# Performance work log

Measured on AMD Instinct MI355X. Metric: run time of the kernel, lower is better.

The kernel has to match this reference:

```python
import jax, jax.numpy as jnp
import numpy as np

B, T, H = 32, 2048, 1024

def setup_inputs() -> dict:
    key = jax.random.key(0)
    k1, k2, k3 = jax.random.split(key, 3)
    gru_output = jax.random.normal(k1, (B, T, H), dtype=jnp.float32)
    # Xavier uniform bounds
    lim_w = float(np.sqrt(6.0 / (H + H)))
    lim_c = float(np.sqrt(6.0 / (H + 1)))
    attention_weights = jax.random.uniform(k2, (H, H), minval=-lim_w, maxval=lim_w, dtype=jnp.float32)
    context_vector = jax.random.uniform(k3, (H, 1), minval=-lim_c, maxval=lim_c, dtype=jnp.float32)
    return {"gru_output": gru_output, "attention_weights": attention_weights, "context_vector": context_vector}

def reference(gru_output, attention_weights, context_vector):
    # score: [B, T, H]
    score = jnp.tanh(jnp.einsum('bth,hk->btk', gru_output, attention_weights))
    # logits: [B, T]
    logits = jnp.einsum('bth,h->bt', score, context_vector[:, 0])
    attn = jax.nn.softmax(logits, axis=1)  # over time dim
    # context: [B, H]
    context = jnp.einsum('bth,bt->bh', gru_output, attn)
    return (context, attn)
```

## Files before the change

kernel.cpp:

```cpp
#include <hip/hip_runtime.h>
#include <hip/hip_bf16.h>
#include <stdint.h>

#define B_DIM 32
#define T_DIM 2048
#define H_DIM 1024
#define M_DIM (B_DIM * T_DIM)
#define K_DIM H_DIM
#define N_DIM H_DIM

#define BM 256
#define BN 256
#define BKT 32
#define NTILES (K_DIM / BKT)
#define DEPTH 3

typedef __attribute__((ext_vector_type(4))) float f32x4;
typedef __attribute__((ext_vector_type(8))) short short8;
typedef __attribute__((ext_vector_type(4))) short short4v;

__device__ __forceinline__ unsigned short f2bf(float x) {
  unsigned u = __float_as_uint(x);
  return (unsigned short)((u + 0x7FFFu + ((u >> 16) & 1u)) >> 16);
}
__device__ __forceinline__ float bf2f(unsigned short h) {
  return __uint_as_float(((unsigned)h) << 16);
}
__device__ __forceinline__ float fast_tanh(float x) {
  float e = __expf(2.f * x);
  return 1.f - 2.f / (e + 1.f);
}
__device__ __forceinline__ int swz(int r, int s) {
  return ((r >> 1) << 7) + (((((r & 1) << 2) | s) ^ ((r >> 1) & 7)) << 4);
}

__global__ void convert_g_kernel(const float* __restrict__ in,
                                 unsigned short* __restrict__ out) {
  size_t nvec = (size_t)M_DIM * K_DIM / 8;
  size_t stride = (size_t)gridDim.x * blockDim.x;
  for (size_t i = (size_t)blockIdx.x * blockDim.x + threadIdx.x; i < nvec;
       i += stride) {
    const float4* p = (const float4*)(in + i * 8);
    float4 u0 = p[0], u1 = p[1];
    short8 s;
    s[0] = (short)f2bf(u0.x); s[1] = (short)f2bf(u0.y);
    s[2] = (short)f2bf(u0.z); s[3] = (short)f2bf(u0.w);
    s[4] = (short)f2bf(u1.x); s[5] = (short)f2bf(u1.y);
    s[6] = (short)f2bf(u1.z); s[7] = (short)f2bf(u1.w);
    *(short8*)(out + i * 8) = s;
  }
}

__global__ void convert_w_kernel(const float* __restrict__ w,
                                 unsigned short* __restrict__ wt) {
  __shared__ float tile[64][65];
  int n0 = blockIdx.x * 64;
  int k0 = blockIdx.y * 64;
  int j = threadIdx.x & 63;
  int i0 = threadIdx.x >> 6;
#pragma unroll
  for (int ii = 0; ii < 16; ++ii) {
    int i = i0 * 16 + ii;
    tile[i][j] = w[(size_t)(k0 + i) * H_DIM + n0 + j];
  }
  __syncthreads();
#pragma unroll
  for (int ii = 0; ii < 16; ++ii) {
    int i = i0 * 16 + ii;
    wt[(size_t)(n0 + i) * H_DIM + k0 + j] = f2bf(tile[j][i]);
  }
}

__global__ __launch_bounds__(512, 2) void gemm_tanh_logits(
    const unsigned short* __restrict__ A,
    const unsigned short* __restrict__ Bt,
    const float* __restrict__ cvec,
    float* __restrict__ logits) {
  __shared__ unsigned short lds[4 * 16384];

  const int tid = threadIdx.x;
  const int wid = tid >> 6;
  const int lane = tid & 63;

  int p = blockIdx.x;
  int logical = (p & 7) * 128 + (p >> 3);
  int mrow = logical >> 2;
  int ncol = logical & 3;

  const unsigned short* Ap = A + (size_t)mrow * BM * K_DIM;
  const unsigned short* Bp = Bt + (size_t)ncol * BN * K_DIM;

  const unsigned short *gA[2], *gB[2];
#pragma unroll
  for (int j = 0; j < 2; ++j) {
    int o = j * 8192 + tid * 16;
    int pr = o >> 7;
    int v = ((o >> 4) & 7) ^ (pr & 7);
    int r = (pr << 1) | (v >> 2);
    int s = v & 3;
    gA[j] = Ap + (size_t)r * K_DIM + s * 8;
    gB[j] = Bp + (size_t)r * K_DIM + s * 8;
  }
  const int ldst0 = wid * 512;
  const int ldst1 = wid * 512 + 4096;

  auto stageA = [&](int tt, int bi) {
    __builtin_amdgcn_global_load_lds(
        (const __attribute__((address_space(1))) unsigned int*)(gA[0] + tt * BKT),
        (__attribute__((address_space(3))) unsigned int*)(lds + bi * 16384 + ldst0),
        16, 0, 0);
    __builtin_amdgcn_global_load_lds(
        (const __attribute__((address_space(1))) unsigned int*)(gA[1] + tt * BKT),
        (__attribute__((address_space(3))) unsigned int*)(lds + bi * 16384 + ldst1),
        16, 0, 0);
  };
  auto stageB = [&](int tt, int bi) {
    __builtin_amdgcn_global_load_lds(
        (const __attribute__((address_space(1))) unsigned int*)(gB[0] + tt * BKT),
        (__attribute__((address_space(3))) unsigned int*)(lds + bi * 16384 + 8192 + ldst0),
        16, 0, 0);
    __builtin_amdgcn_global_load_lds(
        (const __attribute__((address_space(1))) unsigned int*)(gB[1] + tt * BKT),
        (__attribute__((address_space(3))) unsigned int*)(lds + bi * 16384 + 8192 + ldst1),
        16, 0, 0);
  };

  const int wm = wid >> 2;
  const int wn = wid & 3;
  const int fr = lane & 15;
  const int sl = lane >> 4;

  const int aoff = swz(wm * 128 + fr, sl) >> 1;
  const int boff = (swz(wn * 64 + fr, sl) >> 1) + 8192;

  f32x4 acc[8][4];
#pragma unroll
  for (int m = 0; m < 8; ++m)
#pragma unroll
    for (int n = 0; n < 4; ++n) acc[m][n] = (f32x4){0.f, 0.f, 0.f, 0.f};

  stageA(0, 0); stageB(0, 0);
  stageA(1, 1); stageB(1, 1);
  stageA(2, 2); stageB(2, 2);
  asm volatile("s_waitcnt vmcnt(8)" ::: "memory");
  __builtin_amdgcn_s_barrier();

  for (int T = 0; T < NTILES; T += 4) {
#pragma unroll
    for (int u = 0; u < 4; ++u) {
      const int t = T + u;
      const unsigned short* L0 = lds + u * 16384;
      short8 a[4], b[4], a2[4];
#pragma unroll
      for (int m = 0; m < 4; ++m) a[m] = *(const short8*)(L0 + aoff + m * 512);
#pragma unroll
      for (int n = 0; n < 4; ++n) b[n] = *(const short8*)(L0 + boff + n * 512);
      if (t + DEPTH < NTILES) stageA(t + DEPTH, (u + 3) & 3);
      __builtin_amdgcn_sched_barrier(0);
      __builtin_amdgcn_s_barrier();
      asm volatile("s_waitcnt lgkmcnt(0)" ::: "memory");
      __builtin_amdgcn_sched_barrier(0);
      __builtin_amdgcn_s_setprio(1);
#pragma unroll
      for (int m = 0; m < 4; ++m)
#pragma unroll
        for (int n = 0; n < 4; ++n)
          acc[m][n] = __builtin_amdgcn_mfma_f32_16x16x32_bf16(a[m], b[n],
                                                              acc[m][n], 0, 0, 0);
      __builtin_amdgcn_s_setprio(0);
      __builtin_amdgcn_sched_barrier(0);
      __builtin_amdgcn_s_barrier();
#pragma unroll
      for (int m = 0; m < 4; ++m)
        a2[m] = *(const short8*)(L0 + aoff + (m + 4) * 512);
      if (t + DEPTH < NTILES) stageB(t + DEPTH, (u + 3) & 3);
      __builtin_amdgcn_sched_barrier(0);
      __builtin_amdgcn_s_barrier();
      asm volatile("s_waitcnt lgkmcnt(0)" ::: "memory");
      __builtin_amdgcn_sched_barrier(0);
      __builtin_amdgcn_s_setprio(1);
#pragma unroll
      for (int m = 0; m < 4; ++m)
#pragma unroll
        for (int n = 0; n < 4; ++n)
          acc[m + 4][n] = __builtin_amdgcn_mfma_f32_16x16x32_bf16(
              a2[m], b[n], acc[m + 4][n], 0, 0, 0);
      __builtin_amdgcn_s_setprio(0);
      __builtin_amdgcn_sched_barrier(0);
      if (t < NTILES - DEPTH)
        asm volatile("s_waitcnt vmcnt(8)" ::: "memory");
      else if (t == NTILES - DEPTH)
        asm volatile("s_waitcnt vmcnt(4)" ::: "memory");
      else if (t == NTILES - 2)
        asm volatile("s_waitcnt vmcnt(0)" ::: "memory");
      __builtin_amdgcn_s_barrier();
    }
  }

  const int cgrp = lane >> 4;
  const int cidx = lane & 15;
  const int colb = ncol * BN + wn * 64;
  const int rowb = mrow * BM + wm * 128;
  float cw[4];
#pragma unroll
  for (int n = 0; n < 4; ++n) cw[n] = cvec[colb + n * 16 + cidx];
#pragma unroll
  for (int m = 0; m < 8; ++m) {
    float s0 = 0.f, s1 = 0.f, s2 = 0.f, s3 = 0.f;
#pragma unroll
    for (int n = 0; n < 4; ++n) {
      s0 += fast_tanh(acc[m][n][0]) * cw[n];
      s1 += fast_tanh(acc[m][n][1]) * cw[n];
      s2 += fast_tanh(acc[m][n][2]) * cw[n];
      s3 += fast_tanh(acc[m][n][3]) * cw[n];
    }
#pragma unroll
    for (int mask = 1; mask < 16; mask <<= 1) {
      s0 += __shfl_xor(s0, mask);
      s1 += __shfl_xor(s1, mask);
      s2 += __shfl_xor(s2, mask);
      s3 += __shfl_xor(s3, mask);
    }
    if (cidx == 0) {
      int row = rowb + m * 16 + cgrp * 4;
      atomicAdd(&logits[row + 0], s0);
      atomicAdd(&logits[row + 1], s1);
      atomicAdd(&logits[row + 2], s2);
      atomicAdd(&logits[row + 3], s3);
    }
  }
}

__global__ void softmax_kernel(float* __restrict__ la) {
  int b = blockIdx.x;
  float* row = la + (size_t)b * T_DIM;
  int tid = threadIdx.x;
  int wid = tid >> 6, lane = tid & 63;
  __shared__ float red[4];

  float v[8];
  float mx = -3.4e38f;
#pragma unroll
  for (int i = 0; i < 8; ++i) {
    v[i] = row[tid + i * 256];
    mx = fmaxf(mx, v[i]);
  }
#pragma unroll
  for (int mask = 32; mask >= 1; mask >>= 1) mx = fmaxf(mx, __shfl_xor(mx, mask));
  if (lane == 0) red[wid] = mx;
  __syncthreads();
  mx = fmaxf(fmaxf(red[0], red[1]), fmaxf(red[2], red[3]));
  __syncthreads();

  float sum = 0.f;
#pragma unroll
  for (int i = 0; i < 8; ++i) {
    v[i] = __expf(v[i] - mx);
    sum += v[i];
  }
#pragma unroll
  for (int mask = 32; mask >= 1; mask >>= 1) sum += __shfl_xor(sum, mask);
  if (lane == 0) red[wid] = sum;
  __syncthreads();
  sum = red[0] + red[1] + red[2] + red[3];
  float inv = 1.f / sum;
#pragma unroll
  for (int i = 0; i < 8; ++i) row[tid + i * 256] = v[i] * inv;
}

__global__ void context_kernel(const unsigned short* __restrict__ Gb,
                               const float* __restrict__ attn,
                               float* __restrict__ ctx) {
  int tc = blockIdx.x;
  int b = blockIdx.y;
  int h = threadIdx.x * 4;
  const unsigned short* g = Gb + ((size_t)b * T_DIM + tc * 128) * H_DIM + h;
  const float* a = attn + b * T_DIM + tc * 128;
  float s0 = 0.f, s1 = 0.f, s2 = 0.f, s3 = 0.f;
#pragma unroll 4
  for (int t = 0; t < 128; ++t) {
    short4v v = *(const short4v*)(g + (size_t)t * H_DIM);
    float w = a[t];
    s0 += w * bf2f((unsigned short)v[0]);
    s1 += w * bf2f((unsigned short)v[1]);
    s2 += w * bf2f((unsigned short)v[2]);
    s3 += w * bf2f((unsigned short)v[3]);
  }
  float* cb = ctx + b * H_DIM + h;
  atomicAdd(cb + 0, s0);
  atomicAdd(cb + 1, s1);
  atomicAdd(cb + 2, s2);
  atomicAdd(cb + 3, s3);
}

extern "C" void kernel_launch(void* const* d_in, const int* in_sizes, int n_in,
                              void* d_out, int out_size, void* d_ws, size_t ws_size,
                              hipStream_t stream) {
  const float* G = (const float*)d_in[0];
  const float* W = (const float*)d_in[1];
  const float* c = (const float*)d_in[2];
  float* out = (float*)d_out;
  float* ctx = out;
  float* attn = out + B_DIM * H_DIM;

  unsigned short* Gb = (unsigned short*)d_ws;
  unsigned short* Wt = (unsigned short*)((char*)d_ws +
                                         (size_t)M_DIM * K_DIM * 2);

  hipMemsetAsync(d_out, 0, (size_t)out_size * sizeof(float), stream);

  convert_g_kernel<<<4096, 256, 0, stream>>>(G, Gb);
  convert_w_kernel<<<dim3(16, 16), 256, 0, stream>>>(W, Wt);
  gemm_tanh_logits<<<1024, 512, 0, stream>>>(Gb, Wt, c, attn);
  softmax_kernel<<<B_DIM, 256, 0, stream>>>(attn);
  context_kernel<<<dim3(16, 32), 256, 0, stream>>>(Gb, attn, ctx);
}
```

Measured before the change: 565.8 us.

## Double-buffer LDS fragment registers in GEMM main loop and widen context loads

The GEMM inner loop now preloads the next tile's A/B fragments into a second register set while the current tile's MFMAs run. This cuts the per-tile barriers from three to one and removes the lgkmcnt stall before the first MFMA half. The context kernel switches to 8-wide bf16 loads, with each 256-thread block covering two 128-row time chunks, which halves the grid. The cost is higher register pressure from the extra fragment buffers, plus a risk of LDS read/write hazards now that fewer barriers separate staging from reads.

```diff
diff --git a/kernel.cpp b/kernel.cpp
--- a/kernel.cpp
+++ b/kernel.cpp
@@ -17,7 +17,6 @@
 
 typedef __attribute__((ext_vector_type(4))) float f32x4;
 typedef __attribute__((ext_vector_type(8))) short short8;
-typedef __attribute__((ext_vector_type(4))) short short4v;
 
 __device__ __forceinline__ unsigned short f2bf(float x) {
   unsigned u = __float_as_uint(x);
@@ -139,61 +138,63 @@
 #pragma unroll
     for (int n = 0; n < 4; ++n) acc[m][n] = (f32x4){0.f, 0.f, 0.f, 0.f};
 
+  short8 ra[2][4], rb[2][4];
+
   stageA(0, 0); stageB(0, 0);
   stageA(1, 1); stageB(1, 1);
   stageA(2, 2); stageB(2, 2);
   asm volatile("s_waitcnt vmcnt(8)" ::: "memory");
   __builtin_amdgcn_s_barrier();
+#pragma unroll
+  for (int m = 0; m < 4; ++m) ra[0][m] = *(const short8*)(lds + aoff + m * 512);
+#pragma unroll
+  for (int n = 0; n < 4; ++n) rb[0][n] = *(const short8*)(lds + boff + n * 512);
 
   for (int T = 0; T < NTILES; T += 4) {
 #pragma unroll
     for (int u = 0; u < 4; ++u) {
       const int t = T + u;
+      const int cs = u & 1, ns = cs ^ 1;
       const unsigned short* L0 = lds + u * 16384;
-      short8 a[4], b[4], a2[4];
-#pragma unroll
-      for (int m = 0; m < 4; ++m) a[m] = *(const short8*)(L0 + aoff + m * 512);
-#pragma unroll
-      for (int n = 0; n < 4; ++n) b[n] = *(const short8*)(L0 + boff + n * 512);
+      const unsigned short* L1 = lds + ((u + 1) & 3) * 16384;
+      short8 rx[4];
+#pragma unroll
+      for (int m = 0; m < 4; ++m)
+        rx[m] = *(const short8*)(L0 + aoff + (m + 4) * 512);
       if (t + DEPTH < NTILES) stageA(t + DEPTH, (u + 3) & 3);
-      __builtin_amdgcn_sched_barrier(0);
-      __builtin_amdgcn_s_barrier();
-      asm volatile("s_waitcnt lgkmcnt(0)" ::: "memory");
-      __builtin_amdgcn_sched_barrier(0);
       __builtin_amdgcn_s_setprio(1);
 #pragma unroll
       for (int m = 0; m < 4; ++m)
 #pragma unroll
         for (int n = 0; n < 4; ++n)
-          acc[m][n] = __builtin_amdgcn_mfma_f32_16x16x32_bf16(a[m], b[n],
-                                                              acc[m][n], 0, 0, 0);
+          acc[m][n] = __builtin_amdgcn_mfma_f32_16x16x32_bf16(
+              ra[cs][m], rb[cs][n], acc[m][n], 0, 0, 0);
       __builtin_amdgcn_s_setprio(0);
-      __builtin_amdgcn_sched_barrier(0);
-      __builtin_amdgcn_s_barrier();
-#pragma unroll
-      for (int m = 0; m < 4; ++m)
-        a2[m] = *(const short8*)(L0 + aoff + (m + 4) * 512);
       if (t + DEPTH < NTILES) stageB(t + DEPTH, (u + 3) & 3);
-      __builtin_amdgcn_sched_barrier(0);
-      __builtin_amdgcn_s_barrier();
-      asm volatile("s_waitcnt lgkmcnt(0)" ::: "memory");
-      __builtin_amdgcn_sched_barrier(0);
-      __builtin_amdgcn_s_setprio(1);
-#pragma unroll
-      for (int m = 0; m < 4; ++m)
-#pragma unroll
-        for (int n = 0; n < 4; ++n)
-          acc[m + 4][n] = __builtin_amdgcn_mfma_f32_16x16x32_bf16(
-              a2[m], b[n], acc[m + 4][n], 0, 0, 0);
-      __builtin_amdgcn_s_setprio(0);
-      __builtin_amdgcn_sched_barrier(0);
       if (t < NTILES - DEPTH)
         asm volatile("s_waitcnt vmcnt(8)" ::: "memory");
       else if (t == NTILES - DEPTH)
         asm volatile("s_waitcnt vmcnt(4)" ::: "memory");
       else if (t == NTILES - 2)
         asm volatile("s_waitcnt vmcnt(0)" ::: "memory");
+      asm volatile("s_waitcnt lgkmcnt(0)" ::: "memory");
       __builtin_amdgcn_s_barrier();
+      if (t + 1 < NTILES) {
+#pragma unroll
+        for (int m = 0; m < 4; ++m)
+          ra[ns][m] = *(const short8*)(L1 + aoff + m * 512);
+#pragma unroll
+        for (int n = 0; n < 4; ++n)
+          rb[ns][n] = *(const short8*)(L1 + boff + n * 512);
+      }
+      __builtin_amdgcn_s_setprio(1);
+#pragma unroll
+      for (int m = 0; m < 4; ++m)
+#pragma unroll
+        for (int n = 0; n < 4; ++n)
+          acc[m + 4][n] = __builtin_amdgcn_mfma_f32_16x16x32_bf16(
+              rx[m], rb[cs][n], acc[m + 4][n], 0, 0, 0);
+      __builtin_amdgcn_s_setprio(0);
     }
   }
 
@@ -273,24 +274,24 @@
                                float* __restrict__ ctx) {
   int tc = blockIdx.x;
   int b = blockIdx.y;
-  int h = threadIdx.x * 4;
-  const unsigned short* g = Gb + ((size_t)b * T_DIM + tc * 128) * H_DIM + h;
-  const float* a = attn + b * T_DIM + tc * 128;
-  float s0 = 0.f, s1 = 0.f, s2 = 0.f, s3 = 0.f;
+  int th = threadIdx.x >> 7;
+  int h = (threadIdx.x & 127) * 8;
+  const unsigned short* g =
+      Gb + ((size_t)b * T_DIM + tc * 256 + th * 128) * H_DIM + h;
+  const float* a = attn + b * T_DIM + tc * 256 + th * 128;
+  float s[8];
+#pragma unroll
+  for (int j = 0; j < 8; ++j) s[j] = 0.f;
 #pragma unroll 4
   for (int t = 0; t < 128; ++t) {
-    short4v v = *(const short4v*)(g + (size_t)t * H_DIM);
+    short8 v = *(const short8*)(g + (size_t)t * H_DIM);
     float w = a[t];
-    s0 += w * bf2f((unsigned short)v[0]);
-    s1 += w * bf2f((unsigned short)v[1]);
-    s2 += w * bf2f((unsigned short)v[2]);
-    s3 += w * bf2f((unsigned short)v[3]);
+#pragma unroll
+    for (int j = 0; j < 8; ++j) s[j] += w * bf2f((unsigned short)v[j]);
   }
   float* cb = ctx + b * H_DIM + h;
-  atomicAdd(cb + 0, s0);
-  atomicAdd(cb + 1, s1);
-  atomicAdd(cb + 2, s2);
-  atomicAdd(cb + 3, s3);
+#pragma unroll
+  for (int j = 0; j < 8; ++j) atomicAdd(cb + j, s[j]);
 }
 
 extern "C" void kernel_launch(void* const* d_in, const int* in_sizes, int n_in,
@@ -313,5 +314,5 @@
   convert_w_kernel<<<dim3(16, 16), 256, 0, stream>>>(W, Wt);
   gemm_tanh_logits<<<1024, 512, 0, stream>>>(Gb, Wt, c, attn);
   softmax_kernel<<<B_DIM, 256, 0, stream>>>(attn);
-  context_kernel<<<dim3(16, 32), 256, 0, stream>>>(Gb, attn, ctx);
-}
+  context_kernel<<<dim3(8, 32), 256, 0, stream>>>(Gb, attn, ctx);
+}
```

Result: slower. 793.9 us (+40.3%).
